# Optimization experiments

Measured on AMD Instinct MI355X. Metric: run time of the kernel, lower is better.

## Reference

```python
import jax, jax.numpy as jnp
import numpy as np

B, T, N, D, H, NMASK = 8192, 2, 40, 64, 1, 3
EPS = 1e-5


def setup_inputs() -> dict:
    key = jax.random.key(0)
    ks = jax.random.split(key, 12)
    F = T * N * 2 * D  # flattened feature size fed to BatchNorm1d
    return {
        "x": jax.random.normal(ks[0], (B, N, D), jnp.float32),
        "masker": jax.random.uniform(ks[1], (T, NMASK, N, N), jnp.float32, -0.27, 0.27),  # xavier-like
        "ln_gamma": jnp.ones((N,), jnp.float32),
        "ln_beta": jnp.zeros((N,), jnp.float32),
        "gnn_w": jax.random.normal(ks[2], (1, T, H, 2 * D, D), jnp.float32) * 0.05,
        "gnn_b": jax.random.normal(ks[3], (T, H, N, D), jnp.float32) * 0.05,
        "bn_gamma": jnp.ones((H, F), jnp.float32),
        "bn_beta": jnp.zeros((H, F), jnp.float32),
        "bn_mean": jax.random.normal(ks[4], (H, F), jnp.float32) * 0.1,
        "bn_var": jax.random.uniform(ks[5], (H, F), jnp.float32, 0.5, 1.5),
        "gate_w": jax.random.normal(ks[6], (N * D, N), jnp.float32) * 0.02,
        "gate_b": jnp.zeros((N,), jnp.float32),
    }


def reference(x, masker, ln_gamma, ln_beta, gnn_w, gnn_b, bn_gamma, bn_beta, bn_mean, bn_var, gate_w, gate_b):
    b = x.shape[0]
    # broadcast input to towers: (B, T, N, D)
    h = jnp.broadcast_to(x[:, None], (b, T, N, D))
    # adjacency from product of mask matrices: (T, N, N)
    adj = jax.nn.relu(jnp.prod(masker, axis=1))
    mask = (adj != 0).astype(x.dtype)
    # LayerNorm(num_fields) applied on transposed adj == normalize over rows (axis -2)
    mu = adj.mean(axis=-2, keepdims=True)
    var = adj.var(axis=-2, keepdims=True)
    ln = (adj - mu) / jnp.sqrt(var + EPS) * ln_gamma[:, None] + ln_beta[:, None]
    x_masked = ln + (1.0 - mask) * (-1e9) + jnp.eye(N, dtype=x.dtype)
    # softmax over rows (dim=1 of (T,N,N)) then re-mask
    A = jax.nn.softmax(x_masked, axis=1) * mask  # (T, N, N)
    for idx in range(H):
        # nei[b,t,n,d] = sum_m h[b,t,m,d] * A[t,m,n]
        nei = jnp.einsum('btmd,tmn->btnd', h, A)
        hc = jnp.concatenate([h, nei], axis=-1)  # (B,T,N,2D)
        flat = hc.reshape(b, -1)
        flat = (flat - bn_mean[idx]) / jnp.sqrt(bn_var[idx] + EPS) * bn_gamma[idx] + bn_beta[idx]
        hc = flat.reshape(b, T, N, 2 * D)
        # per-tower transform: (B,T,N,2D) x (T,2D,D) -> (B,T,N,D)
        h = jnp.einsum('btnf,tfd->btnd', hc, gnn_w[0, :, idx]) + gnn_b[:, idx]
    # attention pooling over fields
    logits = h.reshape(b, T, N * D) @ gate_w + gate_b  # (B,T,N)
    w = jax.nn.softmax(logits, axis=2)
    return jnp.sum(h * w[..., None], axis=2)  # (B, T, D)
```

## Files before the change

### kernel.cpp

```cpp
#include <hip/hip_runtime.h>
#include <hip/hip_bf16.h>
#include <stdint.h>

typedef float v4f __attribute__((ext_vector_type(4)));
typedef short v8s __attribute__((ext_vector_type(8)));

#define NB 40

__device__ __forceinline__ unsigned short f2b(float f) {
  __hip_bfloat16 h = __float2bfloat16(f);
  unsigned short u;
  __builtin_memcpy(&u, &h, 2);
  return u;
}
__device__ __forceinline__ unsigned pk2(float lo, float hi) {
  __hip_bfloat162 h = __float22bfloat162_rn(make_float2(lo, hi));
  unsigned u;
  __builtin_memcpy(&u, &h, 4);
  return u;
}
__device__ __forceinline__ float b2f16(unsigned short h) {
  return __uint_as_float(((unsigned)h) << 16);
}
__device__ __forceinline__ float blo(unsigned u) { return __uint_as_float(u << 16); }
__device__ __forceinline__ float bhi(unsigned u) { return __uint_as_float(u & 0xFFFF0000u); }


__global__ __launch_bounds__(256) void prep(
    const float* __restrict__ masker,
    const float* __restrict__ ln_gamma, const float* __restrict__ ln_beta,
    const float* __restrict__ gnn_w, const float* __restrict__ gnn_b,
    const float* __restrict__ bn_gamma, const float* __restrict__ bn_beta,
    const float* __restrict__ bn_mean, const float* __restrict__ bn_var,
    const float* __restrict__ gate_w,
    unsigned short* __restrict__ A1pk, unsigned short* __restrict__ W2pk,
    unsigned short* __restrict__ Gpk, float* __restrict__ s1,
    float* __restrict__ sNT, float* __restrict__ bias2T)
{
  const int tid = threadIdx.x;
  if (blockIdx.x == 0) {
    __shared__ float AtL[2 * NB * NB];
    for (int col = tid; col < 2 * NB; col += 256) {
      int t = col / NB, n = col % NB;
      float adj[NB];
      for (int m = 0; m < NB; ++m) {
        float p = masker[((t*3+0)*NB+m)*NB+n]
                * masker[((t*3+1)*NB+m)*NB+n]
                * masker[((t*3+2)*NB+m)*NB+n];
        adj[m] = p > 0.f ? p : 0.f;
      }
      float mu = 0.f;
      for (int m = 0; m < NB; ++m) mu += adj[m];
      mu *= (1.f/NB);
      float var = 0.f;
      for (int m = 0; m < NB; ++m) { float dv = adj[m]-mu; var += dv*dv; }
      var *= (1.f/NB);
      float inv = rsqrtf(var + 1e-5f);
      float xm[NB]; float mx = -3e38f;
      for (int m = 0; m < NB; ++m) {
        float lnv = (adj[m]-mu)*inv*ln_gamma[m] + ln_beta[m];
        float v = lnv + (adj[m] != 0.f ? 0.f : -1e9f) + (m==n ? 1.f : 0.f);
        xm[m] = v; mx = fmaxf(mx, v);
      }
      float ssum = 0.f;
      for (int m = 0; m < NB; ++m) { xm[m] = __expf(xm[m]-mx); ssum += xm[m]; }
      float isum = 1.f/ssum;
      for (int m = 0; m < NB; ++m)
        AtL[(t*NB+n)*NB+m] = (adj[m] != 0.f) ? xm[m]*isum : 0.f;
    }
    __syncthreads();
    for (int e = tid; e < 6144; e += 256) {
      int frag = e >> 9, rem = e & 511, lane = rem >> 3, jj = rem & 7;
      int t = frag / 6, r2 = frag % 6, nt = r2 >> 1, ks = r2 & 1;
      int n = nt*16 + (lane & 15);
      int m = ks*32 + (lane >> 4)*8 + jj;
      A1pk[e] = f2b((n < NB && m < NB) ? AtL[(t*NB+n)*NB+m] : 0.f);
    }
  } else {
    const int gid = (blockIdx.x - 1) * 256 + tid, gsz = 63 * 256;
    for (int e = gid; e < 16384; e += gsz) {
      int frag = e >> 9, rem = e & 511, lane = rem >> 3, jj = rem & 7;
      int t = frag >> 4, ks = (frag >> 2) & 3, dt = frag & 3;
      int f = ks*32 + (lane >> 4)*8 + jj, d = dt*16 + (lane & 15);
      W2pk[e] = f2b(gnn_w[t*8192 + f*64 + d]);
    }
    for (int e = gid; e < 122880; e += gsz) {
      int frag = e >> 9, rem = e & 511, lane = rem >> 3, jj = rem & 7;
      int kt = frag / 3, jt = frag % 3;
      int fl = kt*32 + (lane >> 4)*8 + jj, j = jt*16 + (lane & 15);
      Gpk[e] = f2b(j < NB ? gate_w[fl*NB + j] : 0.f);
    }
    for (int e = gid; e < 5120; e += gsz) {
      int t = e / 2560, n = (e % 2560) / 64, d = e & 63;
      int F = (t*NB + n)*128 + d;
      s1[e] = bn_gamma[F] * rsqrtf(bn_var[F] + 1e-5f);
    }
    for (int e = gid; e < 5120; e += gsz) {
      int t = e / 2560, d = (e % 2560) / 40, n = e % 40;
      int F = (t*NB + n)*128 + 64 + d;
      sNT[e] = bn_gamma[F] * rsqrtf(bn_var[F] + 1e-5f);
    }
    for (int e4 = gid; e4 < 20480; e4 += gsz) {
      int e = e4 >> 2, part = e4 & 3;
      int t = e / 2560, d = (e % 2560) / 40, n = e % 40;
      float acc = (part == 0) ? gnn_b[(t*NB + n)*64 + d] : 0.f;
      int Fb = (t*NB + n)*128;
      int f0 = part * 32;
      for (int f = f0; f < f0 + 32; ++f) {
        float s = bn_gamma[Fb+f] * rsqrtf(bn_var[Fb+f] + 1e-5f);
        float o = bn_beta[Fb+f] - bn_mean[Fb+f] * s;
        acc += o * gnn_w[t*8192 + f*64 + d];
      }
      acc += __shfl_xor(acc, 1);
      acc += __shfl_xor(acc, 2);
      if (part == 0) bias2T[e] = acc;
    }
  }
}

__global__ __launch_bounds__(256, 3) void kernelM(
    const float* __restrict__ x,
    const unsigned short* __restrict__ A1pk, const unsigned short* __restrict__ W2pk,
    const unsigned short* __restrict__ Gpk, const float* __restrict__ s1,
    const float* __restrict__ sNT, const float* __restrict__ bias2T,
    const float* __restrict__ gate_b, float* __restrict__ out)
{
  __shared__ __align__(16) unsigned short hc[160 * 136];
  __shared__ float pj[16 * 48];

  const int tid = threadIdx.x;
  const int lane = tid & 63;
  const int w = tid >> 6;
  const int l = lane & 15, q = lane >> 4;
  const int b0 = blockIdx.x * 4;
  unsigned* hcU = (unsigned*)hc;
  unsigned short* hL = hc;

  uint4 xr[5];
  #pragma unroll
  for (int it = 0; it < 5; ++it) {
    const int c = it * 256 + tid, row = c >> 3, dp8 = c & 7;
    const float* xp = x + (size_t)b0 * 2560 + row * 64 + dp8 * 8;
    const float4 f0 = *(const float4*)xp;
    const float4 f1 = *(const float4*)(xp + 4);
    xr[it] = make_uint4(pk2(f0.x, f0.y), pk2(f0.z, f0.w),
                        pk2(f1.x, f1.y), pk2(f1.z, f1.w));
  }
  if (tid < 12) hcU[5120 + tid] = 0u;
  #pragma unroll
  for (int it = 0; it < 5; ++it) {
    const int c = it * 256 + tid, row = c >> 3, dp8 = c & 7;
    const int bq = row / NB, n = row - bq * NB;
    unsigned short* base = hc + (bq * 64 + dp8 * 8) * NB + n;
    const unsigned uu0 = xr[it].x, uu1 = xr[it].y, uu2 = xr[it].z, uu3 = xr[it].w;
    base[0*NB] = (unsigned short)(uu0 & 0xFFFF);
    base[1*NB] = (unsigned short)(uu0 >> 16);
    base[2*NB] = (unsigned short)(uu1 & 0xFFFF);
    base[3*NB] = (unsigned short)(uu1 >> 16);
    base[4*NB] = (unsigned short)(uu2 & 0xFFFF);
    base[5*NB] = (unsigned short)(uu2 >> 16);
    base[6*NB] = (unsigned short)(uu3 & 0xFFFF);
    base[7*NB] = (unsigned short)(uu3 >> 16);
  }
  __syncthreads();
  v8s b1[4][2];
  #pragma unroll
  for (int i = 0; i < 4; ++i)
    #pragma unroll
    for (int ks = 0; ks < 2; ++ks)
      b1[i][ks] = *(const v8s*)(hc + ((w * 4 + i) * 16 + l) * NB + ks * 32 + q * 8);
  __syncthreads();

  #pragma unroll
  for (int t = 0; t < 2; ++t) {
    if (t) __syncthreads();

    v8s a1[3][2], w2[4];
    #pragma unroll
    for (int nt = 0; nt < 3; ++nt)
      #pragma unroll
      for (int ks = 0; ks < 2; ++ks)
        a1[nt][ks] = *(const v8s*)(A1pk + (((t*3 + nt)*2 + ks) << 9) + lane*8);
    #pragma unroll
    for (int ks = 0; ks < 4; ++ks)
      w2[ks] = *(const v8s*)(W2pk + (((t*4 + ks)*4 + w) << 9) + lane*8);

    #pragma unroll
    for (int it = 0; it < 5; ++it) {
      const int c = it*256 + tid;
      const int row = c >> 3, dp8 = c & 7;
      const uint4 xv = xr[it];
      const int n = row % NB;
      const float4 sA = *(const float4*)(s1 + (t*NB + n)*64 + dp8*8);
      const float4 sB = *(const float4*)(s1 + (t*NB + n)*64 + dp8*8 + 4);
      uint4 p;
      p.x = pk2(blo(xv.x)*sA.x, bhi(xv.x)*sA.y);
      p.y = pk2(blo(xv.y)*sA.z, bhi(xv.y)*sA.w);
      p.z = pk2(blo(xv.z)*sB.x, bhi(xv.z)*sB.y);
      p.w = pk2(blo(xv.w)*sB.z, bhi(xv.w)*sB.w);
      *(uint4*)(hcU + row*68 + dp8*4) = p;
    }
    #pragma unroll
    for (int i = 0; i < 4; ++i) {
      const int R = (w*4+i)*16 + l;
      const int bb = R >> 6, d = R & 63;
      #pragma unroll
      for (int nt = 0; nt < 3; ++nt) {
        v4f acc = {0.f, 0.f, 0.f, 0.f};
        acc = __builtin_amdgcn_mfma_f32_16x16x32_bf16(a1[nt][0], b1[i][0], acc, 0, 0, 0);
        acc = __builtin_amdgcn_mfma_f32_16x16x32_bf16(a1[nt][1], b1[i][1], acc, 0, 0, 0);
        const float4 sv = *(const float4*)(sNT + (t*64+d)*40 + nt*16 + q*4);
        #pragma unroll
        for (int r = 0; r < 4; ++r) {
          int n = nt*16 + q*4 + r;
          if (n < NB) hc[(bb*NB + n)*136 + 64 + d] = f2b(acc[r]*sv[r]);
        }
      }
    }
    __syncthreads();
    unsigned pkr0[10], pkr1[10];
    #pragma unroll
    for (int mt = 0; mt < 10; ++mt) {
      v4f acc = {0.f, 0.f, 0.f, 0.f};
      #pragma unroll
      for (int ks = 0; ks < 4; ++ks) {
        v8s af = *(const v8s*)(hc + (mt*16 + l)*136 + ks*32 + q*8);
        acc = __builtin_amdgcn_mfma_f32_16x16x32_bf16(af, w2[ks], acc, 0, 0, 0);
      }
      const int d = w*16 + l;
      const int G = mt*16 + q*4;
      const int bb = G / NB, n0 = G - bb*NB;
      const float4 bv = *(const float4*)(bias2T + (t*64+d)*40 + n0);
      pkr0[mt] = pk2(acc[0] + bv.x, acc[1] + bv.y);
      pkr1[mt] = pk2(acc[2] + bv.z, acc[3] + bv.w);
    }
    __syncthreads();
    #pragma unroll
    for (int mt = 0; mt < 10; ++mt) {
      const int d = w*16 + l;
      const int G = mt*16 + q*4;
      const int bb = G / NB, n0 = G - bb*NB;
      hL[bb*2568 + (n0+0)*64 + d] = (unsigned short)(pkr0[mt] & 0xFFFF);
      hL[bb*2568 + (n0+1)*64 + d] = (unsigned short)(pkr0[mt] >> 16);
      hL[bb*2568 + (n0+2)*64 + d] = (unsigned short)(pkr1[mt] & 0xFFFF);
      hL[bb*2568 + (n0+3)*64 + d] = (unsigned short)(pkr1[mt] >> 16);
    }
    __syncthreads();
    v4f ac0 = {0,0,0,0}, ac1 = {0,0,0,0}, ac2 = {0,0,0,0};
    for (int kt = w; kt < 80; kt += 4) {
      v8s bf = *(const v8s*)(hL + (l & 3)*2568 + kt*32 + q*8);
      v8s g0 = *(const v8s*)(Gpk + ((kt*3+0) << 9) + lane*8);
      v8s g1 = *(const v8s*)(Gpk + ((kt*3+1) << 9) + lane*8);
      v8s g2 = *(const v8s*)(Gpk + ((kt*3+2) << 9) + lane*8);
      ac0 = __builtin_amdgcn_mfma_f32_16x16x32_bf16(g0, bf, ac0, 0, 0, 0);
      ac1 = __builtin_amdgcn_mfma_f32_16x16x32_bf16(g1, bf, ac1, 0, 0, 0);
      ac2 = __builtin_amdgcn_mfma_f32_16x16x32_bf16(g2, bf, ac2, 0, 0, 0);
    }
    if (l < 4) {
      #pragma unroll
      for (int r = 0; r < 4; ++r) {
        pj[(w*4 + l)*48 +  0 + q*4 + r] = ac0[r];
        pj[(w*4 + l)*48 + 16 + q*4 + r] = ac1[r];
        pj[(w*4 + l)*48 + 32 + q*4 + r] = ac2[r];
      }
    }
    __syncthreads();
    {
      float v = -3.0e38f;
      if (lane < NB) {
        v = gate_b[lane];
        #pragma unroll
        for (int ww = 0; ww < 4; ++ww) v += pj[(ww*4 + w)*48 + lane];
      }
      float mx = v;
      #pragma unroll
      for (int m = 1; m < 64; m <<= 1) mx = fmaxf(mx, __shfl_xor(mx, m));
      float e = (lane < NB) ? __expf(v - mx) : 0.f;
      float es = e;
      #pragma unroll
      for (int m = 1; m < 64; m <<= 1) es += __shfl_xor(es, m);
      const float wgt = e / es;
      float accp = 0.f;
      #pragma unroll
      for (int n = 0; n < NB; ++n)
        accp += b2f16(hL[w*2568 + n*64 + lane]) * __shfl(wgt, n);
      out[((size_t)(b0 + w)*2 + t)*64 + lane] = accp;
    }
  }
}

extern "C" void kernel_launch(void* const* d_in, const int* in_sizes, int n_in,
                              void* d_out, int out_size, void* d_ws, size_t ws_size,
                              hipStream_t stream) {
  const float* x        = (const float*)d_in[0];
  const float* masker   = (const float*)d_in[1];
  const float* ln_gamma = (const float*)d_in[2];
  const float* ln_beta  = (const float*)d_in[3];
  const float* gnn_w    = (const float*)d_in[4];
  const float* gnn_b    = (const float*)d_in[5];
  const float* bn_gamma = (const float*)d_in[6];
  const float* bn_beta  = (const float*)d_in[7];
  const float* bn_mean  = (const float*)d_in[8];
  const float* bn_var   = (const float*)d_in[9];
  const float* gate_w   = (const float*)d_in[10];
  const float* gate_b   = (const float*)d_in[11];
  float* out = (float*)d_out;

  char* ws = (char*)d_ws;
  unsigned short* A1pk   = (unsigned short*)(ws + 0);
  unsigned short* W2pk   = (unsigned short*)(ws + 12288);
  unsigned short* Gpk    = (unsigned short*)(ws + 45056);
  float*          s1     = (float*)(ws + 290816);
  float*          sNT    = (float*)(ws + 311296);
  float*          bias2T = (float*)(ws + 331904);

  prep<<<64, 256, 0, stream>>>(masker, ln_gamma, ln_beta, gnn_w, gnn_b,
                               bn_gamma, bn_beta, bn_mean, bn_var, gate_w,
                               A1pk, W2pk, Gpk, s1, sNT, bias2T);
  kernelM<<<2048, 256, 0, stream>>>(x, A1pk, W2pk, Gpk,
                                    s1, sNT, bias2T, gate_b, out);
}
```

Baseline: 276.8 us.

## Parallelize adjacency softmax across wave lanes and relax kernelM launch bounds

The block-0 prep path now gives each adjacency column to one 64-lane wavefront, with one lane per row, instead of running it serially in a single thread. Mean, variance, max and sum become butterfly shuffle reductions, which shortens the serial critical path of the prep kernel. Separately, the main kernel's min-blocks-per-SM hint of 3 is dropped, so the compiler may use more registers at the cost of lower occupancy.

```diff
diff --git a/kernel.cpp b/kernel.cpp
--- a/kernel.cpp
+++ b/kernel.cpp
@@ -40,40 +40,49 @@
   const int tid = threadIdx.x;
   if (blockIdx.x == 0) {
     __shared__ float AtL[2 * NB * NB];
-    for (int col = tid; col < 2 * NB; col += 256) {
-      int t = col / NB, n = col % NB;
-      float adj[NB];
-      for (int m = 0; m < NB; ++m) {
+    const int w = tid >> 6, lane = tid & 63;
+    #pragma unroll 1
+    for (int it = 0; it < 20; ++it) {
+      const int c = it * 4 + w;
+      const int t = c / NB, n = c % NB;
+      const int m = lane;
+      float adj = 0.f;
+      if (m < NB) {
         float p = masker[((t*3+0)*NB+m)*NB+n]
                 * masker[((t*3+1)*NB+m)*NB+n]
                 * masker[((t*3+2)*NB+m)*NB+n];
-        adj[m] = p > 0.f ? p : 0.f;
-      }
-      float mu = 0.f;
-      for (int m = 0; m < NB; ++m) mu += adj[m];
-      mu *= (1.f/NB);
-      float var = 0.f;
-      for (int m = 0; m < NB; ++m) { float dv = adj[m]-mu; var += dv*dv; }
-      var *= (1.f/NB);
-      float inv = rsqrtf(var + 1e-5f);
-      float xm[NB]; float mx = -3e38f;
-      for (int m = 0; m < NB; ++m) {
-        float lnv = (adj[m]-mu)*inv*ln_gamma[m] + ln_beta[m];
-        float v = lnv + (adj[m] != 0.f ? 0.f : -1e9f) + (m==n ? 1.f : 0.f);
-        xm[m] = v; mx = fmaxf(mx, v);
-      }
-      float ssum = 0.f;
-      for (int m = 0; m < NB; ++m) { xm[m] = __expf(xm[m]-mx); ssum += xm[m]; }
-      float isum = 1.f/ssum;
-      for (int m = 0; m < NB; ++m)
-        AtL[(t*NB+n)*NB+m] = (adj[m] != 0.f) ? xm[m]*isum : 0.f;
+        adj = p > 0.f ? p : 0.f;
+      }
+      float s = adj;
+      #pragma unroll
+      for (int d = 1; d < 64; d <<= 1) s += __shfl_xor(s, d);
+      const float mu = s * (1.f/NB);
+      const float dv = (m < NB) ? adj - mu : 0.f;
+      float v2 = dv * dv;
+      #pragma unroll
+      for (int d = 1; d < 64; d <<= 1) v2 += __shfl_xor(v2, d);
+      const float inv = rsqrtf(v2 * (1.f/NB) + 1e-5f);
+      float val = -3.0e38f;
+      if (m < NB) {
+        float lnv = dv * inv * ln_gamma[m] + ln_beta[m];
+        val = lnv + (adj != 0.f ? 0.f : -1e9f) + (m == n ? 1.f : 0.f);
+      }
+      float mx = val;
+      #pragma unroll
+      for (int d = 1; d < 64; d <<= 1) mx = fmaxf(mx, __shfl_xor(mx, d));
+      const float e = (m < NB) ? __expf(val - mx) : 0.f;
+      float es = e;
+      #pragma unroll
+      for (int d = 1; d < 64; d <<= 1) es += __shfl_xor(es, d);
+      if (m < NB)
+        AtL[(t*NB+n)*NB + m] = (adj != 0.f) ? e / es : 0.f;
     }
     __syncthreads();
     for (int e = tid; e < 6144; e += 256) {
-      int frag = e >> 9, rem = e & 511, lane = rem >> 3, jj = rem & 7;
+      int frag = e >> 9, rem = e & 511, lane2 = rem >> 3, jj = rem & 7;
       int t = frag / 6, r2 = frag % 6, nt = r2 >> 1, ks = r2 & 1;
-      int n = nt*16 + (lane & 15);
-      int m = ks*32 + (lane >> 4)*8 + jj;
+      int n = nt*16 + (lane2 & 15);
+      int m = ks*32 + (lane2 >> 4)*8 + jj;
       A1pk[e] = f2b((n < NB && m < NB) ? AtL[(t*NB+n)*NB+m] : 0.f);
     }
   } else {
@@ -118,7 +127,7 @@
   }
 }
 
-__global__ __launch_bounds__(256, 3) void kernelM(
+__global__ __launch_bounds__(256) void kernelM(
     const float* __restrict__ x,
     const unsigned short* __restrict__ A1pk, const unsigned short* __restrict__ W2pk,
     const unsigned short* __restrict__ Gpk, const float* __restrict__ s1,
```

New measurement: 239.8 us. 1.15x faster.
